# Kernel optimization log

Hardware: AMD Instinct MI355X
Metric: run time of the kernel (lower is better)

Reference implementation:

```python
import jax, jax.numpy as jnp
import numpy as np

TEMPERATURE = 8.0  # sqrt(d_k=64)

def setup_inputs() -> dict:
    key = jax.random.key(0)
    ks = jax.random.split(key, 6)
    shape = (16, 2048, 64)  # [batch*heads, seq_len, d_k]
    names = ["q_real", "k_real", "v_real", "q_phase", "k_phase", "v_phase"]
    return {n: jax.random.normal(k, shape, dtype=jnp.float32) for n, k in zip(names, ks)}

def reference(q_real, k_real, v_real, q_phase, k_phase, v_phase):
    # Complex QK^T scores: (q_r + i q_p)(k_r + i k_p)^H-style split used by the module
    attn_real = jnp.einsum('bqd,bkd->bqk', q_real, k_real) - jnp.einsum('bqd,bkd->bqk', q_phase, k_phase)
    attn_phase = jnp.einsum('bqd,bkd->bqk', q_real, k_phase) + jnp.einsum('bqd,bkd->bqk', q_phase, k_real)
    # continue_complex=True path, mask=None, dropout in eval (p effectively 0)
    attn_real = jax.nn.softmax(attn_real / TEMPERATURE, axis=2)
    attn_phase = jax.nn.softmax(attn_phase / TEMPERATURE, axis=2)
    output_real = jnp.einsum('bqk,bkd->bqd', attn_real, v_real) - jnp.einsum('bqk,bkd->bqd', attn_phase, v_phase)
    output_phase = jnp.einsum('bqk,bkd->bqd', attn_real, v_phase) + jnp.einsum('bqk,bkd->bqd', attn_phase, v_real)
    return output_real, output_phase, attn_real
```

## Files before the change

kernel.cpp:

```cpp
#include <hip/hip_runtime.h>
#include <hip/hip_bf16.h>
#include <stdint.h>

#define BATCH 16
#define SEQ   2048
#define DK    64
#define BQ    (BATCH * SEQ)
#define MAT   ((size_t)BQ * DK)

typedef float  f32x4  __attribute__((ext_vector_type(4)));
typedef __bf16 bf16x8 __attribute__((ext_vector_type(8)));
typedef unsigned short u16x8 __attribute__((ext_vector_type(8)));
typedef unsigned short u16x4 __attribute__((ext_vector_type(4)));

#define MFMA16(a, b, c) __builtin_amdgcn_mfma_f32_16x16x32_bf16((a), (b), (c), 0, 0, 0)

#define TILEU 16384

__device__ __forceinline__ unsigned short bfbits(float f) {
  return __builtin_bit_cast(unsigned short, __float2bfloat16(f));
}

__device__ __forceinline__ void cvt_store(unsigned short* dst, f32x4 a, f32x4 c) {
  u16x8 v;
  v[0] = bfbits(a[0]); v[1] = bfbits(a[1]); v[2] = bfbits(a[2]); v[3] = bfbits(a[3]);
  v[4] = bfbits(c[0]); v[5] = bfbits(c[1]); v[6] = bfbits(c[2]); v[7] = bfbits(c[3]);
  *(u16x8*)dst = v;
}

__device__ __forceinline__ bf16x8 ldbf(const unsigned short* p) {
  return __builtin_bit_cast(bf16x8, *(const u16x8*)p);
}

__device__ __forceinline__ void gload16(const unsigned short* g, unsigned short* l) {
  __builtin_amdgcn_global_load_lds(
      (const __attribute__((address_space(1))) void*)g,
      (__attribute__((address_space(3))) void*)l, 16, 0, 0);
}

__global__ __launch_bounds__(256)
void ck_prep(const float* __restrict__ kr, const float* __restrict__ kp,
             const float* __restrict__ vr, const float* __restrict__ vp,
             const float* __restrict__ qr, const float* __restrict__ qp,
             unsigned short* __restrict__ kv, unsigned short* __restrict__ qb)
{
  __shared__ __align__(16) unsigned short VL[8192];
  const int tid = threadIdx.x;

  if (blockIdx.x >= BATCH * 32) {
    const size_t i8 = ((size_t)(blockIdx.x - BATCH * 32) * 256 + tid) * 8;
    const float* src = (i8 < MAT) ? qr : qp;
    const size_t off = (i8 < MAT) ? i8 : i8 - MAT;
    f32x4 a = *(const f32x4*)(src + off);
    f32x4 c = *(const f32x4*)(src + off + 4);
    cvt_store(qb + i8, a, c);
    return;
  }

  const int b = blockIdx.x >> 5, tile = blockIdx.x & 31;
  unsigned short* blk = kv + (size_t)(b * 32 + tile) * TILEU;
  const size_t go = ((size_t)b * SEQ + tile * 64) * DK;

  {
    const int row = tid >> 2, cp = tid & 3, sw = row & 7;
    const int c0 = cp * 2, c1 = cp * 2 + 1;
    const float* gr = kr + go + (size_t)row * DK + cp * 16;
    f32x4 r0 = ((const f32x4*)gr)[0], r1 = ((const f32x4*)gr)[1];
    f32x4 r2 = ((const f32x4*)gr)[2], r3 = ((const f32x4*)gr)[3];
    const float* gp = kp + go + (size_t)row * DK + cp * 16;
    f32x4 p0 = ((const f32x4*)gp)[0], p1 = ((const f32x4*)gp)[1];
    f32x4 p2 = ((const f32x4*)gp)[2], p3 = ((const f32x4*)gp)[3];
    cvt_store(blk + row * 64 + (c0 ^ sw) * 8, r0, r1);
    cvt_store(blk + row * 64 + (c1 ^ sw) * 8, r2, r3);
    cvt_store(blk + 4096 + row * 64 + (c0 ^ sw) * 8, p0, p1);
    cvt_store(blk + 4096 + row * 64 + (c1 ^ sw) * 8, p2, p3);
  }
  {
    const int key = tid & 15, d0 = (tid >> 4) * 4;
    #pragma unroll
    for (int pass = 0; pass < 4; ++pass) {
      const int kk = pass * 16 + key;
      f32x4 a = *(const f32x4*)(vr + go + (size_t)kk * DK + d0);
      f32x4 c = *(const f32x4*)(vp + go + (size_t)kk * DK + d0);
      const int kc = kk >> 3, kl = kk & 7;
      #pragma unroll
      for (int j = 0; j < 4; ++j) {
        const int d = d0 + j;
        VL[d * 64 + (kc ^ (d & 7)) * 8 + kl]        = bfbits(a[j]);
        VL[4096 + d * 64 + (kc ^ (d & 7)) * 8 + kl] = bfbits(c[j]);
      }
    }
  }
  __syncthreads();
  #pragma unroll
  for (int it = 0; it < 4; ++it)
    *(u16x8*)(blk + 8192 + it * 2048 + tid * 8) = *(const u16x8*)(VL + it * 2048 + tid * 8);
}

__global__ __launch_bounds__(256, 4)
void ck_sums(const unsigned short* __restrict__ qb,
             const unsigned short* __restrict__ kv, float* __restrict__ wsums)
{
  __shared__ __align__(16) unsigned short KT[2][8192];

  const int tid  = threadIdx.x;
  const int wq   = tid >> 6, lane = tid & 63;
  const int lrow = lane & 15, lgrp = lane >> 4;

  const int hw = blockIdx.x;
  const int logical = (hw & 7) * 256 + (hw >> 3);
  const int b = logical >> 7, qtile = (logical >> 2) & 31, slice = logical & 3;

  const int qrow = qtile * 64 + wq * 16 + lrow;
  const size_t qoff = ((size_t)b * SEQ + qrow) * DK;
  bf16x8 aQ0 = ldbf(qb + qoff + lgrp * 8);
  bf16x8 aQ1 = ldbf(qb + qoff + 32 + lgrp * 8);
  bf16x8 aQ2 = ldbf(qb + MAT + qoff + lgrp * 8);
  bf16x8 aQ3 = ldbf(qb + MAT + qoff + 32 + lgrp * 8);

  auto issue = [&](int tile, int buf) {
    const unsigned short* src = kv + (size_t)(b * 32 + tile) * TILEU;
    #pragma unroll
    for (int c = 0; c < 4; ++c) {
      const int ch = wq * 4 + c;
      gload16(src + ch * 512 + lane * 8, &KT[buf][ch * 512]);
    }
  };

  float lsR[4] = {0.f, 0.f, 0.f, 0.f};
  float lsP[4] = {0.f, 0.f, 0.f, 0.f};

  issue(slice * 8 + 0, 0);
  issue(slice * 8 + 1, 1);
  int cur = 0;
  for (int i = 0; i < 8; ++i) {
    if (i < 7) { asm volatile("s_waitcnt vmcnt(4)" ::: "memory"); }
    else       { asm volatile("s_waitcnt vmcnt(0)" ::: "memory"); }
    __builtin_amdgcn_sched_barrier(0);
    __syncthreads();

    const unsigned short* KB = KT[cur];
    #pragma unroll
    for (int t = 0; t < 4; ++t) {
      const int key16 = t * 16 + lrow;
      const int swk = lrow & 7;
      bf16x8 b0 = ldbf(&KB[key16 * 64 + ((lgrp    ) ^ swk) * 8]);
      bf16x8 b1 = ldbf(&KB[key16 * 64 + ((lgrp + 4) ^ swk) * 8]);
      bf16x8 b2 = ldbf(&KB[4096 + key16 * 64 + ((lgrp    ) ^ swk) * 8]);
      bf16x8 b3 = ldbf(&KB[4096 + key16 * 64 + ((lgrp + 4) ^ swk) * 8]);
      f32x4 t1 = {}, t2 = {}, sp = {};
      t1 = MFMA16(aQ0, b0, t1); t1 = MFMA16(aQ1, b1, t1);
      t2 = MFMA16(aQ2, b2, t2); t2 = MFMA16(aQ3, b3, t2);
      sp = MFMA16(aQ0, b2, sp); sp = MFMA16(aQ1, b3, sp);
      sp = MFMA16(aQ2, b0, sp); sp = MFMA16(aQ3, b1, sp);
      #pragma unroll
      for (int r = 0; r < 4; ++r) {
        lsR[r] += __expf((t1[r] - t2[r]) * 0.125f);
        lsP[r] += __expf(sp[r] * 0.125f);
      }
    }
    __syncthreads();
    if (i + 2 < 8) issue(slice * 8 + i + 2, cur);
    cur ^= 1;
  }

  #pragma unroll
  for (int r = 0; r < 4; ++r) {
    float sR = lsR[r], sP = lsP[r];
    #pragma unroll
    for (int m = 1; m < 16; m <<= 1) {
      sR += __shfl_xor(sR, m, 64);
      sP += __shfl_xor(sP, m, 64);
    }
    if (lrow == 0) {
      const size_t row = (size_t)b * SEQ + qtile * 64 + wq * 16 + lgrp * 4 + r;
      wsums[(size_t)(slice * 2 + 0) * BQ + row] = sR;
      wsums[(size_t)(slice * 2 + 1) * BQ + row] = sP;
    }
  }
}

__global__ __launch_bounds__(256, 2)
void ck_main(const unsigned short* __restrict__ qb,
             const unsigned short* __restrict__ kv,
             const float* __restrict__ wsums, float* __restrict__ dout)
{
  __shared__ __align__(16) unsigned short KV[2][16384];
  __shared__ __align__(16) unsigned short Pr[64][32], Pp[64][32];

  const int tid  = threadIdx.x;
  const int wq   = tid >> 6, lane = tid & 63;
  const int lrow = lane & 15, lgrp = lane >> 4;

  const int hw = blockIdx.x;
  const int logical = (hw & 7) * 64 + (hw >> 3);
  const int b = logical >> 5, qtile = logical & 31;

  float* outR = dout;
  float* outP = dout + MAT;
  float* attn = dout + 2 * MAT + ((size_t)b * SEQ + (size_t)qtile * 64) * SEQ;

  const int qrow = qtile * 64 + wq * 16 + lrow;
  const size_t qoff = ((size_t)b * SEQ + qrow) * DK;
  bf16x8 aQ0 = ldbf(qb + qoff + lgrp * 8);
  bf16x8 aQ1 = ldbf(qb + qoff + 32 + lgrp * 8);
  bf16x8 aQ2 = ldbf(qb + MAT + qoff + lgrp * 8);
  bf16x8 aQ3 = ldbf(qb + MAT + qoff + 32 + lgrp * 8);

  const int qloc = wq * 16 + lgrp * 4;
  float iR[4], iP[4];
  {
    const size_t base = (size_t)b * SEQ + qtile * 64 + qloc;
    #pragma unroll
    for (int r = 0; r < 4; ++r) {
      float sR = 0.f, sP = 0.f;
      #pragma unroll
      for (int z = 0; z < 4; ++z) {
        sR += wsums[(size_t)(z * 2 + 0) * BQ + base + r];
        sP += wsums[(size_t)(z * 2 + 1) * BQ + base + r];
      }
      iR[r] = 1.0f / sR;
      iP[r] = 1.0f / sP;
    }
  }

  auto issue = [&](int tile, int buf) {
    const unsigned short* src = kv + (size_t)(b * 32 + tile) * TILEU;
    #pragma unroll
    for (int c = 0; c < 8; ++c) {
      const int ch = wq * 8 + c;
      gload16(src + ch * 512 + lane * 8, &KV[buf][ch * 512]);
    }
  };

  const u16x8 SGN = {0x8000, 0x8000, 0x8000, 0x8000, 0x8000, 0x8000, 0x8000, 0x8000};
  f32x4 accR[4] = {}, accP[4] = {};

  issue(0, 0);
  issue(1, 1);
  int cur = 0;
  for (int i = 0; i < 32; ++i) {
    const int k0 = i * 64;
    if (i == 0)      { asm volatile("s_waitcnt vmcnt(8)"  ::: "memory"); }
    else if (i < 31) { asm volatile("s_waitcnt vmcnt(12)" ::: "memory"); }
    else             { asm volatile("s_waitcnt vmcnt(4)"  ::: "memory"); }
    __builtin_amdgcn_sched_barrier(0);
    __syncthreads();

    const unsigned short* KB = KV[cur];
    #pragma unroll
    for (int h = 0; h < 2; ++h) {
      #pragma unroll
      for (int t = 0; t < 2; ++t) {
        const int key16 = (h * 2 + t) * 16 + lrow;
        const int swk = lrow & 7;
        bf16x8 b0 = ldbf(&KB[key16 * 64 + ((lgrp    ) ^ swk) * 8]);
        bf16x8 b1 = ldbf(&KB[key16 * 64 + ((lgrp + 4) ^ swk) * 8]);
        bf16x8 b2 = ldbf(&KB[4096 + key16 * 64 + ((lgrp    ) ^ swk) * 8]);
        bf16x8 b3 = ldbf(&KB[4096 + key16 * 64 + ((lgrp + 4) ^ swk) * 8]);
        f32x4 t1 = {}, t2 = {}, sp = {};
        t1 = MFMA16(aQ0, b0, t1); t1 = MFMA16(aQ1, b1, t1);
        t2 = MFMA16(aQ2, b2, t2); t2 = MFMA16(aQ3, b3, t2);
        sp = MFMA16(aQ0, b2, sp); sp = MFMA16(aQ1, b3, sp);
        sp = MFMA16(aQ2, b0, sp); sp = MFMA16(aQ3, b1, sp);
        #pragma unroll
        for (int r = 0; r < 4; ++r) {
          const float er = __expf((t1[r] - t2[r]) * 0.125f) * iR[r];
          const float ep = __expf(sp[r] * 0.125f) * iP[r];
          const int row = qloc + r, col = t * 16 + lrow;
          const int pc = ((col >> 3) ^ (row & 3)) * 8 + (col & 7);
          Pr[row][pc] = bfbits(er);
          Pp[row][pc] = bfbits(ep);
        }
      }
      {
        const int prow = wq * 16 + lrow;
        u16x8 uar = *(const u16x8*)&Pr[prow][(lgrp ^ (prow & 3)) * 8];
        u16x8 uap = *(const u16x8*)&Pp[prow][(lgrp ^ (prow & 3)) * 8];
        u16x8 uan = uap ^ SGN;
        bf16x8 apr = __builtin_bit_cast(bf16x8, uar);
        bf16x8 app = __builtin_bit_cast(bf16x8, uap);
        bf16x8 apn = __builtin_bit_cast(bf16x8, uan);
        #pragma unroll
        for (int nt = 0; nt < 4; ++nt) {
          const int d = nt * 16 + lrow;
          const int cv = ((h * 4 + lgrp) ^ (d & 7)) * 8;
          bf16x8 bvr = ldbf(&KB[8192  + d * 64 + cv]);
          bf16x8 bvp = ldbf(&KB[12288 + d * 64 + cv]);
          accR[nt] = MFMA16(apr, bvr, accR[nt]);
          accR[nt] = MFMA16(apn, bvp, accR[nt]);
          accP[nt] = MFMA16(apr, bvp, accP[nt]);
          accP[nt] = MFMA16(app, bvr, accP[nt]);
        }
      }
      {
        const int j8 = lane & 7;
        #pragma unroll
        for (int s = 0; s < 2; ++s) {
          const int arow = wq * 16 + s * 8 + (lane >> 3);
          const int pc = (((j8 >> 1) ^ (arow & 3)) * 8) + (j8 & 1) * 4;
          u16x4 ua = *(const u16x4*)&Pr[arow][pc];
          f32x4 fa;
          #pragma unroll
          for (int q = 0; q < 4; ++q)
            fa[q] = __builtin_bit_cast(float, (unsigned)ua[q] << 16);
          float* dst = attn + (size_t)arow * SEQ + k0 + h * 32 + j8 * 4;
          __builtin_nontemporal_store(fa, (f32x4*)dst);
        }
      }
    }
    __syncthreads();
    if (i + 2 < 32) issue(i + 2, cur);
    cur ^= 1;
  }

  #pragma unroll
  for (int nt = 0; nt < 4; ++nt) {
    const int d = nt * 16 + lrow;
    #pragma unroll
    for (int r = 0; r < 4; ++r) {
      const size_t o = ((size_t)b * SEQ + qtile * 64 + qloc + r) * DK + d;
      outR[o] = accR[nt][r];
      outP[o] = accP[nt][r];
    }
  }
}

extern "C" void kernel_launch(void* const* d_in, const int* in_sizes, int n_in,
                              void* d_out, int out_size, void* d_ws, size_t ws_size,
                              hipStream_t stream)
{
  const float* qr = (const float*)d_in[0];
  const float* kr = (const float*)d_in[1];
  const float* vr = (const float*)d_in[2];
  const float* qp = (const float*)d_in[3];
  const float* kp = (const float*)d_in[4];
  const float* vp = (const float*)d_in[5];
  float* out = (float*)d_out;

  unsigned short* kv = (unsigned short*)d_ws;
  unsigned short* qb = (unsigned short*)((char*)d_ws + (16u << 20));
  float* wsums = (float*)((char*)d_ws + (24u << 20));

  const unsigned qblocks = (unsigned)(2 * MAT / 8 / 256);
  ck_prep<<<BATCH * 32 + qblocks, 256, 0, stream>>>(kr, kp, vr, vp, qr, qp, kv, qb);
  ck_sums<<<4 * 32 * BATCH, 256, 0, stream>>>(qb, kv, wsums);
  ck_main<<<32 * BATCH, 256, 0, stream>>>(qb, kv, wsums, out);
}
```

Baseline: 149.9 us.

## Fold softmax temperature into Q prep and read K directly from global in sums kernel

Q is now pre-scaled by 1/8 when converted to bf16, so the per-element multiply before exp is dropped in both the sums kernel and the main attention kernel. Because 0.125 is a power of two, the bf16 rounding is unchanged. The sums kernel also drops its LDS double-buffered K staging, along with its barriers and waitcnt, and loads K fragments straight from global or L2 memory. This removes shared-memory use and syncs, which may raise occupancy, but each wave now issues uncoalesced-ish global loads and repeats K reads across waves.

New measurement: 156.7 us. 4.5% more time.

```diff
diff --git a/kernel.cpp b/kernel.cpp
--- a/kernel.cpp
+++ b/kernel.cpp
@@ -53,7 +53,7 @@
     const size_t off = (i8 < MAT) ? i8 : i8 - MAT;
     f32x4 a = *(const f32x4*)(src + off);
     f32x4 c = *(const f32x4*)(src + off + 4);
-    cvt_store(qb + i8, a, c);
+    cvt_store(qb + i8, a * 0.125f, c * 0.125f);
     return;
   }
 
@@ -101,8 +101,6 @@
 void ck_sums(const unsigned short* __restrict__ qb,
              const unsigned short* __restrict__ kv, float* __restrict__ wsums)
 {
-  __shared__ __align__(16) unsigned short KT[2][8192];
-
   const int tid  = threadIdx.x;
   const int wq   = tid >> 6, lane = tid & 63;
   const int lrow = lane & 15, lgrp = lane >> 4;
@@ -118,36 +116,21 @@
   bf16x8 aQ2 = ldbf(qb + MAT + qoff + lgrp * 8);
   bf16x8 aQ3 = ldbf(qb + MAT + qoff + 32 + lgrp * 8);
 
-  auto issue = [&](int tile, int buf) {
-    const unsigned short* src = kv + (size_t)(b * 32 + tile) * TILEU;
-    #pragma unroll
-    for (int c = 0; c < 4; ++c) {
-      const int ch = wq * 4 + c;
-      gload16(src + ch * 512 + lane * 8, &KT[buf][ch * 512]);
-    }
-  };
-
   float lsR[4] = {0.f, 0.f, 0.f, 0.f};
   float lsP[4] = {0.f, 0.f, 0.f, 0.f};
-
-  issue(slice * 8 + 0, 0);
-  issue(slice * 8 + 1, 1);
-  int cur = 0;
+  const int swk = lrow & 7;
+  const int cA = ((lgrp    ) ^ swk) * 8;
+  const int cB = ((lgrp + 4) ^ swk) * 8;
+
   for (int i = 0; i < 8; ++i) {
-    if (i < 7) { asm volatile("s_waitcnt vmcnt(4)" ::: "memory"); }
-    else       { asm volatile("s_waitcnt vmcnt(0)" ::: "memory"); }
-    __builtin_amdgcn_sched_barrier(0);
-    __syncthreads();
-
-    const unsigned short* KB = KT[cur];
+    const unsigned short* KB = kv + (size_t)(b * 32 + slice * 8 + i) * TILEU;
     #pragma unroll
     for (int t = 0; t < 4; ++t) {
-      const int key16 = t * 16 + lrow;
-      const int swk = lrow & 7;
-      bf16x8 b0 = ldbf(&KB[key16 * 64 + ((lgrp    ) ^ swk) * 8]);
-      bf16x8 b1 = ldbf(&KB[key16 * 64 + ((lgrp + 4) ^ swk) * 8]);
-      bf16x8 b2 = ldbf(&KB[4096 + key16 * 64 + ((lgrp    ) ^ swk) * 8]);
-      bf16x8 b3 = ldbf(&KB[4096 + key16 * 64 + ((lgrp + 4) ^ swk) * 8]);
+      const int rowoff = (t * 16 + lrow) * 64;
+      bf16x8 b0 = ldbf(&KB[rowoff + cA]);
+      bf16x8 b1 = ldbf(&KB[rowoff + cB]);
+      bf16x8 b2 = ldbf(&KB[4096 + rowoff + cA]);
+      bf16x8 b3 = ldbf(&KB[4096 + rowoff + cB]);
       f32x4 t1 = {}, t2 = {}, sp = {};
       t1 = MFMA16(aQ0, b0, t1); t1 = MFMA16(aQ1, b1, t1);
       t2 = MFMA16(aQ2, b2, t2); t2 = MFMA16(aQ3, b3, t2);
@@ -155,13 +138,10 @@
       sp = MFMA16(aQ2, b0, sp); sp = MFMA16(aQ3, b1, sp);
       #pragma unroll
       for (int r = 0; r < 4; ++r) {
-        lsR[r] += __expf((t1[r] - t2[r]) * 0.125f);
-        lsP[r] += __expf(sp[r] * 0.125f);
-      }
-    }
-    __syncthreads();
-    if (i + 2 < 8) issue(slice * 8 + i + 2, cur);
-    cur ^= 1;
+        lsR[r] += __expf(t1[r] - t2[r]);
+        lsP[r] += __expf(sp[r]);
+      }
+    }
   }
 
   #pragma unroll
@@ -265,8 +245,8 @@
         sp = MFMA16(aQ2, b0, sp); sp = MFMA16(aQ3, b1, sp);
         #pragma unroll
         for (int r = 0; r < 4; ++r) {
-          const float er = __expf((t1[r] - t2[r]) * 0.125f) * iR[r];
-          const float ep = __expf(sp[r] * 0.125f) * iP[r];
+          const float er = __expf(t1[r] - t2[r]) * iR[r];
+          const float ep = __expf(sp[r]) * iP[r];
           const int row = qloc + r, col = t * 16 + lrow;
           const int pc = ((col >> 3) ^ (row & 3)) * 8 + (col & 7);
           Pr[row][pc] = bfbits(er);
```
